# Kernel tuning notes

Hardware: AMD Instinct MI355X
Metric: run time of the kernel (lower is better)

## Reference

```python
import jax, jax.numpy as jnp
import numpy as np

B, R, T = 16, 400, 400   # batch, ROIs, BOLD length (= feature_nums)
H, Q = 8, 64             # heads, per-head dim
K_DIL = 4                # dilated_parameter_k
N_GCN = 8


def setup_inputs() -> dict:
    key = jax.random.key(0)
    ks = jax.random.split(key, 12)
    s = lambda *sh: 1.0 / np.sqrt(sh[0])
    return {
        "x": jax.random.normal(ks[0], (B, R, T), jnp.float32),
        "Wk": jax.random.normal(ks[1], (T, H * Q), jnp.float32) * s(T),
        "bk": jnp.zeros((H * Q,), jnp.float32),
        "se_W1": jax.random.normal(ks[2], (H, H // 2), jnp.float32) * s(H),
        "se_b1": jnp.zeros((H // 2,), jnp.float32),
        "se_W2": jax.random.normal(ks[3], (H // 2, H), jnp.float32) * s(H // 2),
        "se_b2": jnp.zeros((H,), jnp.float32),
        "gcn_W": jax.random.normal(ks[4], (N_GCN, T, T), jnp.float32) * s(T),
        "gcn_b": jnp.zeros((N_GCN, T), jnp.float32),
        "fuse_w": jax.random.normal(ks[5], (H,), jnp.float32) * s(H),
        "fuse_b": jnp.zeros((), jnp.float32),
        "mlp_W1": jax.random.normal(ks[6], (T, 256), jnp.float32) * s(T),
        "mlp_b1": jnp.zeros((256,), jnp.float32),
        "mlp_W2": jax.random.normal(ks[7], (256, 128), jnp.float32) * s(256),
        "mlp_b2": jnp.zeros((128,), jnp.float32),
        "mlp_W3": jax.random.normal(ks[8], (128, 64), jnp.float32) * s(128),
        "mlp_b3": jnp.zeros((64,), jnp.float32),
        "mlp_W4": jax.random.normal(ks[9], (64, 5), jnp.float32) * s(64),
        "mlp_b4": jnp.zeros((5,), jnp.float32),
    }


def reference(x, Wk, bk, se_W1, se_b1, se_W2, se_b2, gcn_W, gcn_b,
              fuse_w, fuse_b, mlp_W1, mlp_b1, mlp_W2, mlp_b2,
              mlp_W3, mlp_b3, mlp_W4, mlp_b4):
    dt = x.dtype
    # ---- Transformer: Q = K = linear_k(x) (as in source) ----
    qk = (x @ Wk + bk).reshape(B, R, H, Q).transpose(0, 2, 1, 3)  # [B,H,R,Q]
    rel = jnp.einsum('bhrq,bhsq->bhrs', qk, qk) / jnp.sqrt(jnp.asarray(Q, dt))
    rel = jax.nn.softmax(jax.nn.relu(rel), axis=-1)               # [B,H,R,R]
    # ---- SE gate over heads ----
    gap = rel.mean(axis=(2, 3))                                   # [B,H]
    gate = jax.nn.sigmoid(jax.nn.relu(gap @ se_W1 + se_b1) @ se_W2 + se_b2)
    rel = rel * gate[:, :, None, None]
    # ---- dilated mask (deterministic prob<0.8 branch) ----
    idx = jnp.argsort(rel, axis=-1)                               # [B,H,R,R]
    sel = (idx == 0) | ((idx >= 2 ** K_DIL) & (idx < 2 ** K_DIL + 5))
    mask = jnp.minimum(sel.astype(dt) + jnp.eye(R, dtype=dt), 1.0)
    adj = rel * mask                                              # [B,H,R,R]
    feats = jnp.broadcast_to(x[:, None], (B, H, R, T))            # [B,H,R,T]
    for i in range(N_GCN):
        msg = jnp.einsum('bhrs,bhst->bhrt', adj, feats)
        feats = jax.nn.relu(msg @ gcn_W[i] + gcn_b[i]) + feats
    # ---- 1x1 conv fusion over heads ----
    fused = jnp.einsum('bhrt,h->brt', feats, fuse_w) + fuse_b     # [B,R,T]
    # ---- MLP head ----
    h = jax.nn.relu(fused @ mlp_W1 + mlp_b1)
    h = jax.nn.relu(h @ mlp_W2 + mlp_b2)
    h = jax.nn.relu(h @ mlp_W3 + mlp_b3)
    return jax.nn.relu(h @ mlp_W4 + mlp_b4)                       # [B,R,5]
```

## Files before the change

### kernel.cpp

```cpp
#include <hip/hip_runtime.h>
#include <math.h>

namespace {

constexpr int nB = 16, nR = 400, nT = 400, nH = 8, nQ = 64;
constexpr int BH = nB * nH;
constexpr int HQ = nH * nQ;
constexpr int KP = 416;
constexpr int NK = KP / 32;

typedef __attribute__((ext_vector_type(8))) short short8;
typedef __attribute__((ext_vector_type(4))) float floatx4;

__device__ __forceinline__ unsigned short f2bf(float f) {
  unsigned int u = __float_as_uint(f);
  unsigned int r = (u + 0x7fffu + ((u >> 16) & 1u)) >> 16;
  return (unsigned short)r;
}
__device__ __forceinline__ float bf2f(unsigned short u) {
  return __uint_as_float(((unsigned int)u) << 16);
}

__device__ __forceinline__ void dma16(const void* g, void* l) {
  __builtin_amdgcn_global_load_lds(
      (const __attribute__((address_space(1))) unsigned int*)g,
      (__attribute__((address_space(3))) unsigned int*)l, 16, 0, 0);
}

template<int BM, int BN, int BK, int TM, int TN, bool RELU>
__global__ __launch_bounds__(256) void gemm_k(
    const float* __restrict__ A, const float* __restrict__ W,
    const float* __restrict__ bias,
    float* C, int M, int N, int K)
{
  constexpr int NT = (BM / TM) * (BN / TN);
  static_assert(NT == 256, "block must be 256 threads");
  __shared__ float As[BK][BM + 4];
  __shared__ float Bs[BK][BN + 4];
  const int tid = threadIdx.x;
  const int bm = blockIdx.y * BM;
  const int bn = blockIdx.x * BN;
  const int tx = tid % (BN / TN);
  const int ty = tid / (BN / TN);
  const bool n4ok = ((N & 3) == 0);

  float acc[TM][TN];
#pragma unroll
  for (int i = 0; i < TM; ++i)
#pragma unroll
    for (int j = 0; j < TN; ++j) acc[i][j] = 0.f;

  for (int kt = 0; kt < K; kt += BK) {
#pragma unroll
    for (int i = 0; i < (BM * BK) / (NT * 4); ++i) {
      int flat = (tid + i * NT) * 4;
      int m = flat / BK;
      int k = flat % BK;
      float4 v = *(const float4*)(A + (size_t)(bm + m) * K + kt + k);
      As[k + 0][m] = v.x; As[k + 1][m] = v.y;
      As[k + 2][m] = v.z; As[k + 3][m] = v.w;
    }
#pragma unroll
    for (int i = 0; i < (BK * BN) / (NT * 4); ++i) {
      int flat = (tid + i * NT) * 4;
      int k = flat / BN;
      int n = flat % BN;
      int gn = bn + n;
      float4 v;
      if (n4ok && gn + 3 < N) {
        v = *(const float4*)(W + (size_t)(kt + k) * N + gn);
      } else {
        v.x = (gn + 0 < N) ? W[(size_t)(kt + k) * N + gn + 0] : 0.f;
        v.y = (gn + 1 < N) ? W[(size_t)(kt + k) * N + gn + 1] : 0.f;
        v.z = (gn + 2 < N) ? W[(size_t)(kt + k) * N + gn + 2] : 0.f;
        v.w = (gn + 3 < N) ? W[(size_t)(kt + k) * N + gn + 3] : 0.f;
      }
      *(float4*)&Bs[k][n] = v;
    }
    __syncthreads();
#pragma unroll
    for (int k = 0; k < BK; ++k) {
      float a[TM], b[TN];
#pragma unroll
      for (int i = 0; i < TM; i += 4)
        *(float4*)&a[i] = *(const float4*)&As[k][ty * TM + i];
#pragma unroll
      for (int j = 0; j < TN; j += 4)
        *(float4*)&b[j] = *(const float4*)&Bs[k][tx * TN + j];
#pragma unroll
      for (int i = 0; i < TM; ++i)
#pragma unroll
        for (int j = 0; j < TN; ++j) acc[i][j] += a[i] * b[j];
    }
    __syncthreads();
  }

#pragma unroll
  for (int i = 0; i < TM; ++i) {
    const int gm = bm + ty * TM + i;
    float* crow = C + (size_t)gm * N;
#pragma unroll
    for (int j = 0; j < TN; j += 4) {
      const int gn = bn + tx * TN + j;
      if (n4ok && gn + 3 < N) {
        float4 bv = *(const float4*)(bias + gn);
        float4 v;
        v.x = acc[i][j + 0] + bv.x; v.y = acc[i][j + 1] + bv.y;
        v.z = acc[i][j + 2] + bv.z; v.w = acc[i][j + 3] + bv.w;
        if (RELU) {
          v.x = fmaxf(v.x, 0.f); v.y = fmaxf(v.y, 0.f);
          v.z = fmaxf(v.z, 0.f); v.w = fmaxf(v.w, 0.f);
        }
        *(float4*)(crow + gn) = v;
      } else {
#pragma unroll
        for (int jj = 0; jj < 4; ++jj) {
          int gnn = gn + jj;
          if (gnn < N) {
            float v = acc[i][j + jj] + bias[gnn];
            if (RELU) v = fmaxf(v, 0.f);
            crow[gnn] = v;
          }
        }
      }
    }
  }
}

__global__ __launch_bounds__(256) void gcn_gemm(
    const unsigned short* __restrict__ A,
    const unsigned short* __restrict__ Bt,
    const float* __restrict__ bias,
    unsigned short* __restrict__ Cb,
    const float* __restrict__ x, int first)
{
  __shared__ __align__(16) char smem[36864];

  const int tid = threadIdx.x;
  const int lane = tid & 63;
  const int wave = tid >> 6;

  const int b = blockIdx.x;
  const int xcd = b & 7;
  const int s = b >> 3;
  const int loc = s / 7;
  const int nt = s - loc * 7;
  const int mt = loc * 8 + xcd;
  const int bm = mt * 128;
  const int bn = nt * 64;

  const int wm = (wave & 1) * 64;
  const int wn = (wave >> 1) * 32;

  const unsigned short* gsrc[3];
  int goff[3];
#pragma unroll
  for (int j = 0; j < 3; ++j) {
    const int g = wave * 3 + j;
    if (g < 8) {
      const int row = bm + g * 16 + (lane & 15);
      gsrc[j] = A + (size_t)row * KP + (lane >> 4) * 8;
      goff[j] = g * 1024;
    } else {
      int row = bn + (g - 8) * 16 + (lane & 15);
      if (row > 415) row = 415;
      gsrc[j] = Bt + (size_t)row * KP + (lane >> 4) * 8;
      goff[j] = 8192 + (g - 8) * 1024;
    }
  }

  const int rcol = bn + ((tid & 15) << 2);
  ushort4 resv[2][4];
  if (!first && rcol < nT) {
#pragma unroll
    for (int rh = 0; rh < 2; ++rh)
#pragma unroll
      for (int ii = 0; ii < 4; ++ii) {
        const int gr = bm + rh * 64 + (tid >> 4) + ii * 16;
        resv[rh][ii] = *(const ushort4*)(Cb + (size_t)gr * nT + rcol);
      }
  }

#pragma unroll
  for (int j = 0; j < 3; ++j)
    dma16(gsrc[j], smem + goff[j]);
#pragma unroll
  for (int j = 0; j < 3; ++j)
    dma16(gsrc[j] + 32, smem + 12288 + goff[j]);

  floatx4 acc[4][2] = {};
  const int aoff = (wm >> 4) * 1024;
  const int boff = 8192 + (wn >> 4) * 1024;
  const int lb = lane * 16;

#pragma unroll
  for (int k = 0; k < NK; ++k) {
    if (k == NK - 1)
      asm volatile("s_waitcnt vmcnt(0)" ::: "memory");
    else
      asm volatile("s_waitcnt vmcnt(3)" ::: "memory");
    __builtin_amdgcn_s_barrier();
    __builtin_amdgcn_sched_barrier(0);
    if (k + 2 < NK) {
      char* dst = smem + ((k + 2) % 3) * 12288;
#pragma unroll
      for (int j = 0; j < 3; ++j)
        dma16(gsrc[j] + (k + 2) * 32, dst + goff[j]);
    }
    const char* base = smem + (k % 3) * 12288;
    short8 av[4], bv[2];
#pragma unroll
    for (int mi = 0; mi < 4; ++mi)
      av[mi] = *(const short8*)(base + aoff + mi * 1024 + lb);
#pragma unroll
    for (int ni = 0; ni < 2; ++ni)
      bv[ni] = *(const short8*)(base + boff + ni * 1024 + lb);
#pragma unroll
    for (int mi = 0; mi < 4; ++mi)
#pragma unroll
      for (int ni = 0; ni < 2; ++ni)
        acc[mi][ni] = __builtin_amdgcn_mfma_f32_16x16x32_bf16(
            av[mi], bv[ni], acc[mi][ni], 0, 0, 0);
  }

  float bvv[2];
#pragma unroll
  for (int ni = 0; ni < 2; ++ni) {
    const int col = bn + wn + ni * 16 + (lane & 15);
    bvv[ni] = (col < nT) ? bias[col] : 0.f;
  }

  float* Os = (float*)smem;

  for (int rh = 0; rh < 2; ++rh) {
    __syncthreads();
    if (wm == rh * 64) {
#pragma unroll
      for (int mi = 0; mi < 4; ++mi)
#pragma unroll
        for (int ni = 0; ni < 2; ++ni)
#pragma unroll
          for (int r = 0; r < 4; ++r) {
            const int lrow = mi * 16 + (lane >> 4) * 4 + r;
            const int cl = wn + ni * 16 + (lane & 15);
            Os[lrow * 68 + cl] = fmaxf(acc[mi][ni][r] + bvv[ni], 0.f);
          }
    }
    __syncthreads();

    const int rbase = bm + rh * 64;
#pragma unroll
    for (int ii = 0; ii < 4; ++ii) {
      const int f = tid + ii * 256;
      const int row = f >> 4;
      const int c4 = (f & 15) << 2;
      const int col = bn + c4;
      if (col < nT) {
        const int gr = rbase + row;
        float4 v = *(const float4*)&Os[row * 68 + c4];
        float r0, r1, r2, r3;
        if (first) {
          const int bh = gr / nR;
          const int rr = gr - bh * nR;
          const float* rrow = x + (size_t)(bh >> 3) * (nR * nT) + (size_t)rr * nT;
          float4 rv = *(const float4*)(rrow + col);
          r0 = rv.x; r1 = rv.y; r2 = rv.z; r3 = rv.w;
        } else {
          ushort4 rv = resv[rh][ii];
          r0 = bf2f(rv.x); r1 = bf2f(rv.y); r2 = bf2f(rv.z); r3 = bf2f(rv.w);
        }
        ushort4 o;
        o.x = f2bf(v.x + r0); o.y = f2bf(v.y + r1);
        o.z = f2bf(v.z + r2); o.w = f2bf(v.w + r3);
        *(ushort4*)(Cb + (size_t)gr * nT + col) = o;
      }
    }
  }
}

__global__ void wprep_k(const float* __restrict__ W, unsigned short* __restrict__ Wt)
{
  __shared__ float t[32][33];
  const int i = blockIdx.z;
  const int k0 = blockIdx.x * 32;
  const int n0 = blockIdx.y * 32;
  const int tx = threadIdx.x, ty = threadIdx.y;
#pragma unroll
  for (int r = 0; r < 32; r += 8) {
    int k = k0 + ty + r, n = n0 + tx;
    t[ty + r][tx] = (k < nT && n < nT) ? W[(size_t)i * nT * nT + (size_t)k * nT + n] : 0.f;
  }
  __syncthreads();
#pragma unroll
  for (int r = 0; r < 32; r += 8) {
    int n = n0 + ty + r, k = k0 + tx;
    Wt[(size_t)i * KP * KP + (size_t)n * KP + k] = f2bf(t[tx][ty + r]);
  }
}

__global__ void gate_k(const float* __restrict__ w1, const float* __restrict__ b1,
                       const float* __restrict__ w2, const float* __restrict__ b2,
                       float* gate)
{
  if (threadIdx.x == 0 && blockIdx.x == 0) {
    float h1[4];
    const float gap = 1.0f / 400.0f;
#pragma unroll
    for (int i = 0; i < 4; ++i) {
      float s = b1[i];
      for (int h = 0; h < 8; ++h) s += gap * w1[h * 4 + i];
      h1[i] = fmaxf(s, 0.f);
    }
#pragma unroll
    for (int h = 0; h < 8; ++h) {
      float s = b2[h];
      for (int i = 0; i < 4; ++i) s += h1[i] * w2[i * 8 + h];
      gate[h] = 1.f / (1.f + expf(-s));
    }
  }
}

__global__ __launch_bounds__(256) void qkscore_k(
    const float* __restrict__ qk, float* __restrict__ sc)
{
  __shared__ float Qs[64][68];
  __shared__ float Ks[64][68];

  const int tm = blockIdx.y;
  const int tn = blockIdx.x;
  if (tm > tn) return;

  const int tid = threadIdx.x;
  const int bh = blockIdx.z;
  const int b = bh >> 3, h = bh & 7;
  const int bm = tm * 64;
  const int bn = tn * 64;
  const float* qkb = qk + (size_t)b * nR * HQ + h * nQ;

  {
    const int row = tid & 63;
#pragma unroll
    for (int p = 0; p < 4; ++p) {
      const int kc = (tid >> 6) + p * 4;
      int gr = bm + row; if (gr > 399) gr = 399;
      float4 v = *(const float4*)(qkb + (size_t)gr * HQ + (kc << 2));
      Qs[kc * 4 + 0][row] = v.x; Qs[kc * 4 + 1][row] = v.y;
      Qs[kc * 4 + 2][row] = v.z; Qs[kc * 4 + 3][row] = v.w;
      int gs2 = bn + row; if (gs2 > 399) gs2 = 399;
      float4 w = *(const float4*)(qkb + (size_t)gs2 * HQ + (kc << 2));
      Ks[kc * 4 + 0][row] = w.x; Ks[kc * 4 + 1][row] = w.y;
      Ks[kc * 4 + 2][row] = w.z; Ks[kc * 4 + 3][row] = w.w;
    }
  }
  __syncthreads();

  const int tx = tid & 15;
  const int ty = tid >> 4;
  float acc[4][4] = {};
#pragma unroll 8
  for (int k = 0; k < 64; ++k) {
    float4 a = *(const float4*)&Qs[k][ty * 4];
    float4 bv = *(const float4*)&Ks[k][tx * 4];
    acc[0][0] += a.x * bv.x; acc[0][1] += a.x * bv.y; acc[0][2] += a.x * bv.z; acc[0][3] += a.x * bv.w;
    acc[1][0] += a.y * bv.x; acc[1][1] += a.y * bv.y; acc[1][2] += a.y * bv.z; acc[1][3] += a.y * bv.w;
    acc[2][0] += a.z * bv.x; acc[2][1] += a.z * bv.y; acc[2][2] += a.z * bv.z; acc[2][3] += a.z * bv.w;
    acc[3][0] += a.w * bv.x; acc[3][1] += a.w * bv.y; acc[3][2] += a.w * bv.z; acc[3][3] += a.w * bv.w;
  }

  float* scb = sc + (size_t)bh * nR * 400;

  {
    const int gc = bn + tx * 4;
    if (gc < 400) {
#pragma unroll
      for (int i = 0; i < 4; ++i) {
        const int gr = bm + ty * 4 + i;
        if (gr < 400) {
          float4 o;
          o.x = fmaxf(acc[i][0] * 0.125f, 0.f);
          o.y = fmaxf(acc[i][1] * 0.125f, 0.f);
          o.z = fmaxf(acc[i][2] * 0.125f, 0.f);
          o.w = fmaxf(acc[i][3] * 0.125f, 0.f);
          *(float4*)(scb + (size_t)gr * 400 + gc) = o;
        }
      }
    }
  }

  if (tm != tn) {
    const int gc = bm + ty * 4;
    if (gc < 400) {
#pragma unroll
      for (int j = 0; j < 4; ++j) {
        const int gr = bn + tx * 4 + j;
        if (gr < 400) {
          float4 o;
          o.x = fmaxf(acc[0][j] * 0.125f, 0.f);
          o.y = fmaxf(acc[1][j] * 0.125f, 0.f);
          o.z = fmaxf(acc[2][j] * 0.125f, 0.f);
          o.w = fmaxf(acc[3][j] * 0.125f, 0.f);
          *(float4*)(scb + (size_t)gr * 400 + gc) = o;
        }
      }
    }
  }
}

__global__ __launch_bounds__(256) void rankadj_k(
    const float* __restrict__ sc, const float* __restrict__ gate,
    float* __restrict__ adjval, int* __restrict__ adjcol)
{
  __shared__ float rowbuf[4][408];

  const int wave = threadIdx.x >> 6;
  const int lane = threadIdx.x & 63;
  const int row = blockIdx.x * 4 + wave;
  const int bh = row / nR;
  const int r = row - bh * nR;
  const float* srow = sc + (size_t)row * 400;

  float v[7];
  bool valid[7];
#pragma unroll
  for (int it = 0; it < 7; ++it) {
    const int j = lane + it * 64;
    valid[it] = (j < 400);
    v[it] = valid[it] ? srow[j] : 0.f;
  }

  float m = 0.f;
#pragma unroll
  for (int it = 0; it < 7; ++it) m = fmaxf(m, v[it]);
#pragma unroll
  for (int o = 32; o > 0; o >>= 1) m = fmaxf(m, __shfl_xor(m, o));

  float e[7];
  float s = 0.f;
#pragma unroll
  for (int it = 0; it < 7; ++it) {
    e[it] = valid[it] ? expf(v[it] - m) : 0.f;
    s += e[it];
  }
#pragma unroll
  for (int o = 32; o > 0; o >>= 1) s += __shfl_xor(s, o);

  const float g = gate[bh & 7];
  float val[7];
#pragma unroll
  for (int it = 0; it < 7; ++it) val[it] = (e[it] / s) * g;

#pragma unroll
  for (int it = 0; it < 7; ++it)
    if (valid[it]) rowbuf[wave][lane + it * 64] = val[it];
  __syncthreads();

  const int csp[6] = {0, 16, 17, 18, 19, 20};
  float vc[6];
#pragma unroll
  for (int i = 0; i < 6; ++i) vc[i] = rowbuf[wave][csp[i]];
  int rk[6] = {0, 0, 0, 0, 0, 0};
#pragma unroll
  for (int it = 0; it < 7; ++it) {
    if (valid[it]) {
      const int j = lane + it * 64;
      const float vj = val[it];
#pragma unroll
      for (int i = 0; i < 6; ++i)
        rk[i] += (vj < vc[i]) ? 1 : ((vj == vc[i] && j < csp[i]) ? 1 : 0);
    }
  }
#pragma unroll
  for (int i = 0; i < 6; ++i)
#pragma unroll
    for (int o = 32; o > 0; o >>= 1) rk[i] += __shfl_xor(rk[i], o);

  if (lane == 0) {
    const size_t base = (size_t)row * 8;
    bool dup = false;
#pragma unroll
    for (int i = 0; i < 6; ++i) {
      const int p = rk[i];
      adjcol[base + i] = p;
      adjval[base + i] = rowbuf[wave][p];
      dup = dup || (p == r);
    }
    adjcol[base + 6] = r;
    adjval[base + 6] = dup ? 0.f : rowbuf[wave][r];
    adjcol[base + 7] = r;
    adjval[base + 7] = 0.f;
  }
}

__global__ __launch_bounds__(256) void spmsg_k(
    const int* __restrict__ adjcol, const float* __restrict__ adjval,
    const unsigned short* __restrict__ feats, const float* __restrict__ x,
    int first, unsigned short* __restrict__ msg)
{
  __shared__ unsigned short fs[400 * 20];

  const int tid = threadIdx.x;
  const int bh = blockIdx.x;
  const int c0 = blockIdx.y * 16;

  if (first) {
    const float* src = x + (size_t)(bh >> 3) * (nR * nT);
    for (int i = tid; i < 1600; i += 256) {
      const int r = i >> 2, cg = i & 3;
      const int c = c0 + cg * 4;
      ushort4 o = make_ushort4(0, 0, 0, 0);
      if (c < 400) {
        float4 v = *(const float4*)(src + (size_t)r * nT + c);
        o = make_ushort4(f2bf(v.x), f2bf(v.y), f2bf(v.z), f2bf(v.w));
      }
      *(ushort4*)&fs[r * 20 + cg * 4] = o;
    }
  } else {
    const unsigned short* src = feats + (size_t)bh * nR * nT;
    for (int i = tid; i < 1600; i += 256) {
      const int r = i >> 2, cg = i & 3;
      const int c = c0 + cg * 4;
      ushort4 o = make_ushort4(0, 0, 0, 0);
      if (c < 400) o = *(const ushort4*)(src + (size_t)r * nT + c);
      *(ushort4*)&fs[r * 20 + cg * 4] = o;
    }
  }
  __syncthreads();

  const int* ac = adjcol + (size_t)bh * nR * 8;
  const float* av = adjval + (size_t)bh * nR * 8;
  for (int i = tid; i < 1600; i += 256) {
    const int r = i >> 2, cg = i & 3;
    float a0 = 0.f, a1 = 0.f, a2 = 0.f, a3 = 0.f;
#pragma unroll
    for (int j = 0; j < 7; ++j) {
      const int col = ac[r * 8 + j];
      const float val = av[r * 8 + j];
      ushort4 v = *(const ushort4*)&fs[col * 20 + cg * 4];
      a0 += val * bf2f(v.x); a1 += val * bf2f(v.y);
      a2 += val * bf2f(v.z); a3 += val * bf2f(v.w);
    }
    unsigned short* o = msg + ((size_t)bh * nR + r) * KP + c0 + cg * 4;
    *(ushort4*)o = make_ushort4(f2bf(a0), f2bf(a1), f2bf(a2), f2bf(a3));
  }
}

__global__ void hfuse_k(const unsigned short* __restrict__ feats,
                        const float* __restrict__ fw,
                        const float* __restrict__ fb, float* __restrict__ fused)
{
  size_t i = (size_t)blockIdx.x * 256 + threadIdx.x;
  constexpr size_t tot4 = (size_t)nB * nR * nT / 4;
  if (i >= tot4) return;
  size_t b = i / (nR * nT / 4);
  size_t rem = i % (nR * nT / 4);
  float fbv = fb[0];
  float4 acc = {fbv, fbv, fbv, fbv};
#pragma unroll
  for (int h = 0; h < nH; ++h) {
    float w = fw[h];
    ushort4 v = *(const ushort4*)(feats + ((b * nH + h) * (size_t)(nR * nT / 4) + rem) * 4);
    acc.x += w * bf2f(v.x); acc.y += w * bf2f(v.y);
    acc.z += w * bf2f(v.z); acc.w += w * bf2f(v.w);
  }
  ((float4*)fused)[i] = acc;
}

}

extern "C" void kernel_launch(void* const* d_in, const int* in_sizes, int n_in,
                              void* d_out, int out_size, void* d_ws, size_t ws_size,
                              hipStream_t stream)
{
  (void)in_sizes; (void)n_in; (void)out_size; (void)ws_size;
  const float* x    = (const float*)d_in[0];
  const float* Wk   = (const float*)d_in[1];
  const float* bk   = (const float*)d_in[2];
  const float* seW1 = (const float*)d_in[3];
  const float* seb1 = (const float*)d_in[4];
  const float* seW2 = (const float*)d_in[5];
  const float* seb2 = (const float*)d_in[6];
  const float* gcnW = (const float*)d_in[7];
  const float* gcnb = (const float*)d_in[8];
  const float* fw   = (const float*)d_in[9];
  const float* fb   = (const float*)d_in[10];
  const float* mW1  = (const float*)d_in[11];
  const float* mb1  = (const float*)d_in[12];
  const float* mW2  = (const float*)d_in[13];
  const float* mb2  = (const float*)d_in[14];
  const float* mW3  = (const float*)d_in[15];
  const float* mb3  = (const float*)d_in[16];
  const float* mW4  = (const float*)d_in[17];
  const float* mb4  = (const float*)d_in[18];
  float* out = (float*)d_out;

  float* ws     = (float*)d_ws;
  float* adjval = ws;
  int*   adjcol = (int*)(adjval + 409600);
  float* gate   = (float*)(adjcol + 409600);
  unsigned short* Wt = (unsigned short*)(gate + 64);
  float* qk     = gate + 64 + 692224;
  float* region = qk + (size_t)3276800;
  float* scores = region;
  unsigned short* featsb = (unsigned short*)region;
  unsigned short* msg = (unsigned short*)(region + 10240000);
  float* fused  = (float*)msg;
  float* h1     = fused + (size_t)6400 * 400;
  float* h2     = h1 + (size_t)6400 * 256;
  float* h3     = h2 + (size_t)6400 * 128;

  wprep_k<<<dim3(13, 13, 8), dim3(32, 8), 0, stream>>>(gcnW, Wt);

  gemm_k<64, 64, 16, 4, 4, false><<<dim3(8, 100), 256, 0, stream>>>(
      x, Wk, bk, qk, 6400, 512, 400);

  gate_k<<<1, 64, 0, stream>>>(seW1, seb1, seW2, seb2, gate);

  qkscore_k<<<dim3(7, 7, 128), 256, 0, stream>>>(qk, scores);

  rankadj_k<<<12800, 256, 0, stream>>>(scores, gate, adjval, adjcol);

  for (int i = 0; i < 8; ++i) {
    const int first = (i == 0) ? 1 : 0;
    spmsg_k<<<dim3(BH, 26), 256, 0, stream>>>(adjcol, adjval, featsb, x,
                                              first, msg);
    gcn_gemm<<<dim3(2800), 256, 0, stream>>>(
        msg, Wt + (size_t)i * KP * KP, gcnb + (size_t)i * nT, featsb, x, first);
  }

  hfuse_k<<<2500, 256, 0, stream>>>(featsb, fw, fb, fused);

  gemm_k<64, 64, 16, 4, 4, true><<<dim3(4, 100), 256, 0, stream>>>(
      fused, mW1, mb1, h1, 6400, 256, 400);
  gemm_k<64, 64, 16, 4, 4, true><<<dim3(2, 100), 256, 0, stream>>>(
      h1, mW2, mb2, h2, 6400, 128, 256);
  gemm_k<64, 64, 16, 4, 4, true><<<dim3(1, 100), 256, 0, stream>>>(
      h2, mW3, mb3, h3, 6400, 64, 128);
  gemm_k<64, 64, 16, 4, 4, true><<<dim3(1, 100), 256, 0, stream>>>(
      h3, mW4, mb4, out, 6400, 5, 64);
}
```

Before: 825.2 us.

## Run QK projection and first MLP layer on split-bf16 MFMA GEMM

```diff
diff --git a/kernel.cpp b/kernel.cpp
--- a/kernel.cpp
+++ b/kernel.cpp
@@ -124,6 +124,161 @@
         }
       }
     }
+  }
+}
+
+__global__ void xsplit_k(const float* __restrict__ x,
+                         unsigned short* __restrict__ xh,
+                         unsigned short* __restrict__ xl)
+{
+  int i = blockIdx.x * 256 + threadIdx.x;
+  constexpr int total = 6400 * (KP / 4);
+  if (i >= total) return;
+  int row = i / (KP / 4), cg = i - row * (KP / 4);
+  int c = cg * 4;
+  ushort4 h = make_ushort4(0, 0, 0, 0), l = make_ushort4(0, 0, 0, 0);
+  if (c < 400) {
+    float4 v = *(const float4*)(x + (size_t)row * 400 + c);
+    h.x = f2bf(v.x); l.x = f2bf(v.x - bf2f(h.x));
+    h.y = f2bf(v.y); l.y = f2bf(v.y - bf2f(h.y));
+    h.z = f2bf(v.z); l.z = f2bf(v.z - bf2f(h.z));
+    h.w = f2bf(v.w); l.w = f2bf(v.w - bf2f(h.w));
+  }
+  *(ushort4*)(xh + (size_t)row * KP + c) = h;
+  *(ushort4*)(xl + (size_t)row * KP + c) = l;
+}
+
+__global__ void wksplit_k(const float* __restrict__ W, int N,
+                          unsigned short* __restrict__ Wth,
+                          unsigned short* __restrict__ Wtl)
+{
+  __shared__ float t[32][33];
+  const int k0 = blockIdx.x * 32;
+  const int n0 = blockIdx.y * 32;
+  const int tx = threadIdx.x, ty = threadIdx.y;
+#pragma unroll
+  for (int r = 0; r < 32; r += 8) {
+    int k = k0 + ty + r, n = n0 + tx;
+    t[ty + r][tx] = (k < 400) ? W[(size_t)k * N + n] : 0.f;
+  }
+  __syncthreads();
+#pragma unroll
+  for (int r = 0; r < 32; r += 8) {
+    int n = n0 + ty + r, k = k0 + tx;
+    float v = t[tx][ty + r];
+    unsigned short h = f2bf(v);
+    Wth[(size_t)n * KP + k] = h;
+    Wtl[(size_t)n * KP + k] = f2bf(v - bf2f(h));
+  }
+}
+
+template<bool RELU>
+__global__ __launch_bounds__(256) void sgemm_mfma(
+    const unsigned short* __restrict__ Ah, const unsigned short* __restrict__ Al,
+    const unsigned short* __restrict__ Bh, const unsigned short* __restrict__ Bl,
+    const float* __restrict__ bias,
+    float* __restrict__ C, int N)
+{
+  __shared__ __align__(16) char smem[49152];
+
+  const int tid = threadIdx.x;
+  const int lane = tid & 63;
+  const int wave = tid >> 6;
+
+  const int bm = blockIdx.y * 64;
+  const int bn = blockIdx.x * 64;
+
+  const int wm = (wave & 1) * 32;
+  const int wn = (wave >> 1) * 32;
+
+  const unsigned short* kbase = (wave == 0) ? Ah : (wave == 1) ? Al
+                              : (wave == 2) ? Bh : Bl;
+  const int rbase0 = (wave < 2) ? bm : bn;
+  const unsigned short* gsrc[4];
+  int goff[4];
+#pragma unroll
+  for (int j = 0; j < 4; ++j) {
+    const int row = rbase0 + j * 16 + (lane & 15);
+    gsrc[j] = kbase + (size_t)row * KP + (lane >> 4) * 8;
+    goff[j] = (wave * 4 + j) * 1024;
+  }
+
+#pragma unroll
+  for (int j = 0; j < 4; ++j) dma16(gsrc[j], smem + goff[j]);
+#pragma unroll
+  for (int j = 0; j < 4; ++j) dma16(gsrc[j] + 32, smem + 16384 + goff[j]);
+
+  floatx4 acc[2][2] = {};
+  const int ao = (wm >> 4) * 1024;
+  const int bo = (wn >> 4) * 1024;
+  const int lb = lane * 16;
+
+#pragma unroll
+  for (int k = 0; k < NK; ++k) {
+    if (k == NK - 1)
+      asm volatile("s_waitcnt vmcnt(0)" ::: "memory");
+    else
+      asm volatile("s_waitcnt vmcnt(4)" ::: "memory");
+    __builtin_amdgcn_s_barrier();
+    __builtin_amdgcn_sched_barrier(0);
+    if (k + 2 < NK) {
+      char* dst = smem + ((k + 2) % 3) * 16384;
+#pragma unroll
+      for (int j = 0; j < 4; ++j)
+        dma16(gsrc[j] + (k + 2) * 32, dst + goff[j]);
+    }
+    const char* base = smem + (k % 3) * 16384;
+    short8 ah[2], al[2], bh[2], bl[2];
+#pragma unroll
+    for (int mi = 0; mi < 2; ++mi) {
+      ah[mi] = *(const short8*)(base + ao + mi * 1024 + lb);
+      al[mi] = *(const short8*)(base + 4096 + ao + mi * 1024 + lb);
+    }
+#pragma unroll
+    for (int ni = 0; ni < 2; ++ni) {
+      bh[ni] = *(const short8*)(base + 8192 + bo + ni * 1024 + lb);
+      bl[ni] = *(const short8*)(base + 12288 + bo + ni * 1024 + lb);
+    }
+#pragma unroll
+    for (int mi = 0; mi < 2; ++mi)
+#pragma unroll
+      for (int ni = 0; ni < 2; ++ni) {
+        acc[mi][ni] = __builtin_amdgcn_mfma_f32_16x16x32_bf16(
+            ah[mi], bh[ni], acc[mi][ni], 0, 0, 0);
+        acc[mi][ni] = __builtin_amdgcn_mfma_f32_16x16x32_bf16(
+            ah[mi], bl[ni], acc[mi][ni], 0, 0, 0);
+        acc[mi][ni] = __builtin_amdgcn_mfma_f32_16x16x32_bf16(
+            al[mi], bh[ni], acc[mi][ni], 0, 0, 0);
+      }
+  }
+
+  float* Os = (float*)smem;
+  __syncthreads();
+#pragma unroll
+  for (int mi = 0; mi < 2; ++mi)
+#pragma unroll
+    for (int ni = 0; ni < 2; ++ni)
+#pragma unroll
+      for (int r = 0; r < 4; ++r) {
+        const int lrow = wm + mi * 16 + (lane >> 4) * 4 + r;
+        const int cl = wn + ni * 16 + (lane & 15);
+        Os[lrow * 68 + cl] = acc[mi][ni][r];
+      }
+  __syncthreads();
+
+#pragma unroll
+  for (int ii = 0; ii < 4; ++ii) {
+    const int f = tid + ii * 256;
+    const int row = f >> 4;
+    const int c4 = (f & 15) << 2;
+    float4 v = *(const float4*)&Os[row * 68 + c4];
+    float4 bb = *(const float4*)(bias + bn + c4);
+    v.x += bb.x; v.y += bb.y; v.z += bb.z; v.w += bb.w;
+    if (RELU) {
+      v.x = fmaxf(v.x, 0.f); v.y = fmaxf(v.y, 0.f);
+      v.z = fmaxf(v.z, 0.f); v.w = fmaxf(v.w, 0.f);
+    }
+    *(float4*)(C + (size_t)(bm + row) * N + bn + c4) = v;
   }
 }
 
@@ -608,10 +763,17 @@
   float* h2     = h1 + (size_t)6400 * 256;
   float* h3     = h2 + (size_t)6400 * 128;
 
+  unsigned short* xh  = (unsigned short*)region;
+  unsigned short* xl  = xh + (size_t)6400 * KP;
+  unsigned short* Wth = xl + (size_t)6400 * KP;
+  unsigned short* Wtl = Wth + (size_t)512 * KP;
+
   wprep_k<<<dim3(13, 13, 8), dim3(32, 8), 0, stream>>>(gcnW, Wt);
 
-  gemm_k<64, 64, 16, 4, 4, false><<<dim3(8, 100), 256, 0, stream>>>(
-      x, Wk, bk, qk, 6400, 512, 400);
+  xsplit_k<<<2600, 256, 0, stream>>>(x, xh, xl);
+  wksplit_k<<<dim3(13, 16), dim3(32, 8), 0, stream>>>(Wk, 512, Wth, Wtl);
+  sgemm_mfma<false><<<dim3(8, 100), 256, 0, stream>>>(
+      xh, xl, Wth, Wtl, bk, qk, 512);
 
   gate_k<<<1, 64, 0, stream>>>(seW1, seb1, seW2, seb2, gate);
 
@@ -629,8 +791,11 @@
 
   hfuse_k<<<2500, 256, 0, stream>>>(featsb, fw, fb, fused);
 
-  gemm_k<64, 64, 16, 4, 4, true><<<dim3(4, 100), 256, 0, stream>>>(
-      fused, mW1, mb1, h1, 6400, 256, 400);
+  xsplit_k<<<2600, 256, 0, stream>>>(fused, xh, xl);
+  wksplit_k<<<dim3(13, 8), dim3(32, 8), 0, stream>>>(mW1, 256, Wth, Wtl);
+  sgemm_mfma<true><<<dim3(4, 100), 256, 0, stream>>>(
+      xh, xl, Wth, Wtl, mb1, h1, 256);
+
   gemm_k<64, 64, 16, 4, 4, true><<<dim3(2, 100), 256, 0, stream>>>(
       h1, mW2, mb2, h2, 6400, 128, 256);
   gemm_k<64, 64, 16, 4, 4, true><<<dim3(1, 100), 256, 0, stream>>>(
```

Measured after the change: 821.9 us. About the same (-0.4%).
